# Optimization experiments

Measured on AMD Instinct MI355X. Metric: run time of the kernel, lower is better.

The kernel has to match this reference:

```python
import jax, jax.numpy as jnp
import numpy as np

B = 32768
INPUT_DIM = 2048
D = 2
HIDDEN = 128
V = 20          # output_dim (number of heads)
P = 6           # n_corr_params
R = 10          # r_lora = min(V // 2, 10)


def setup_inputs() -> dict:
    key = jax.random.key(0)
    ks = jax.random.split(key, 12)

    def lin(k, fan_in, shape):
        bound = 1.0 / np.sqrt(fan_in)
        return jax.random.uniform(k, shape, jnp.float32, -bound, bound)

    x = jax.random.normal(ks[0], (B, INPUT_DIM), jnp.float32)
    # encoder: Linear(input_dim, hidden) -> ReLU -> (Dropout=id) -> Linear(hidden, d)
    We1 = lin(ks[1], INPUT_DIM, (INPUT_DIM, HIDDEN))
    be1 = lin(ks[2], INPUT_DIM, (HIDDEN,))
    We2 = lin(ks[3], HIDDEN, (HIDDEN, D))
    be2 = lin(ks[4], HIDDEN, (D,))
    # 20 heads, each Linear(d, hidden) -> ReLU -> Linear(hidden, 6) -> Tanh,
    # stacked into batched weight tensors.
    W1 = lin(ks[5], D, (V, D, HIDDEN))
    b1 = lin(ks[6], D, (V, HIDDEN))
    W2 = lin(ks[7], HIDDEN, (V, HIDDEN, P))
    b2 = lin(ks[8], HIDDEN, (V, P))
    # LoRA params
    lora_A = jax.random.normal(ks[9], (D, R), jnp.float32) * 0.01
    lora_B = jax.random.normal(ks[10], (R, V * P), jnp.float32) * 0.01
    return {"x": x, "We1": We1, "be1": be1, "We2": We2, "be2": be2,
            "W1": W1, "b1": b1, "W2": W2, "b2": b2,
            "lora_A": lora_A, "lora_B": lora_B}


def reference(x, We1, be1, We2, be2, W1, b1, W2, b2, lora_A, lora_B):
    # encoder (nonlinear reduction; dropout is identity in eval)
    z = jax.nn.relu(x @ We1 + be1) @ We2 + be2            # [B, D]
    # all 20 heads as batched GEMMs
    h = jax.nn.relu(jnp.einsum('bd,vdh->bvh', z, W1) + b1)  # [B, V, HIDDEN]
    heads = jnp.tanh(jnp.einsum('bvh,vhp->bvp', h, W2) + b2)  # [B, V, P]
    # LoRA contribution, then outer tanh (note: double tanh, faithful to source)
    lora = (z @ lora_A @ lora_B).reshape(-1, V, P)         # [B, V, P]
    out = jnp.tanh(heads + 0.15 * lora)
    return (out, z)
```

## Files before the change

### kernel.cpp

```cpp
#include <hip/hip_runtime.h>
#include <hip/hip_bf16.h>
#include <cstdint>
#include <cstddef>

#define BDIM   32768
#define KDIM   2048
#define NDIM   128
#define VHEADS 20
#define PDIM   6
#define RLORA  10

#define BK      64
#define NCHUNK  (KDIM / BK)
#define OUT_ELEMS   (BDIM * VHEADS * PDIM)
#define WS_W_BYTES  (KDIM * NDIM * 2)

typedef __attribute__((ext_vector_type(8))) __bf16 bf16x8;
typedef __attribute__((ext_vector_type(4))) float f32x4;
typedef __attribute__((ext_vector_type(2))) float f32x2;
typedef __attribute__((ext_vector_type(4))) unsigned int u32x4;

union FragU { bf16x8 b; u32x4 u; };

__device__ __forceinline__ unsigned int cvt_pk_bf16(float lo, float hi) {
  unsigned int r;
  asm("v_cvt_pk_bf16_f32 %0, %1, %2" : "=v"(r) : "v"(lo), "v"(hi));
  return r;
}

__device__ __forceinline__ void gload_lds16(const void* g, void* l) {
  __builtin_amdgcn_global_load_lds(
      (const __attribute__((address_space(1))) void*)(g),
      (__attribute__((address_space(3))) void*)(l), 16, 0, 0);
}

__device__ __forceinline__ float fast_tanh(float x) {
  float ax = fabsf(x);
  float e  = __expf(-2.0f * ax);
  float t  = __fdividef(1.0f - e, 1.0f + e);
  return copysignf(t, x);
}

#define SBAR() __builtin_amdgcn_sched_barrier(0)
#define GL16(dst, addr, OFFSTR) \
  asm volatile("global_load_dwordx4 %0, %1, off offset:" OFFSTR \
               : "=v"(dst) : "v"(addr))

__global__ __launch_bounds__(256)
void k0_pack(const float* __restrict__ We1,
             const float* __restrict__ lA,
             const float* __restrict__ lB,
             unsigned short* __restrict__ wsw,
             float* __restrict__ wsM) {
  if (blockIdx.x == 128) {
    int t = threadIdx.x;
    if (t < 2 * VHEADS * PDIM) {
      int d  = t / (VHEADS * PDIM);
      int vp = t - d * (VHEADS * PDIM);
      float s = 0.f;
#pragma unroll
      for (int r = 0; r < RLORA; ++r)
        s = fmaf(lA[d * RLORA + r], lB[r * (VHEADS * PDIM) + vp], s);
      wsM[t] = s;
    }
    return;
  }
  int t    = blockIdx.x * 256 + threadIdx.x;
  int lane = t & 63;
  int blk  = t >> 6;
  int ks   = blk & 1;
  int nt   = (blk >> 1) & 7;
  int c    = blk >> 4;
  int n    = nt * 16 + (lane & 15);
  int kb   = c * 64 + ks * 32 + (lane >> 4) * 8;

  unsigned int u[4];
#pragma unroll
  for (int q = 0; q < 4; ++q) {
    float f0 = We1[(size_t)(kb + 2 * q + 0) * NDIM + n];
    float f1 = We1[(size_t)(kb + 2 * q + 1) * NDIM + n];
    __hip_bfloat16 h0 = __float2bfloat16(f0);
    __hip_bfloat16 h1 = __float2bfloat16(f1);
    u[q] = (unsigned int)*reinterpret_cast<unsigned short*>(&h0) |
           ((unsigned int)*reinterpret_cast<unsigned short*>(&h1) << 16);
  }
  *reinterpret_cast<u32x4*>(wsw + (size_t)t * 8) = u32x4{u[0], u[1], u[2], u[3]};
}

__global__ __launch_bounds__(512, 4)
void k1_fused(const float* __restrict__ x,
              const unsigned short* __restrict__ wp,
              const float* __restrict__ be1,
              const float* __restrict__ We2,
              const float* __restrict__ be2,
              const float* __restrict__ W1,
              const float* __restrict__ b1,
              const float* __restrict__ W2,
              const float* __restrict__ b2,
              const float* __restrict__ M,
              float* __restrict__ out,
              float* __restrict__ zout) {
  __shared__ char A0_[16384] __attribute__((aligned(16)));
  __shared__ char A1_[16384] __attribute__((aligned(16)));
  __shared__ float zpart2[64][2][2];
  __shared__ float zsh[64][2];

  const int tid  = threadIdx.x;
  const int lane = tid & 63;
  const int wv   = tid >> 6;
  const int wr   = wv & 3;
  const int wc   = wv >> 2;
  const int l15  = lane & 15;
  const int kgrp = lane >> 4;
  const int blk  = blockIdx.x;

  const char* bwave = (const char*)wp + wc * 8192 + lane * 16 + 4096;

  f32x4 acc[4];
#pragma unroll
  for (int i = 0; i < 4; ++i) acc[i] = f32x4{0.f, 0.f, 0.f, 0.f};

  auto STAGE_A = [&](char* Ad, int c) {
#pragma unroll
    for (int q = 0; q < 2; ++q) {
      int s = tid + q * 512;
      int row = s >> 4;
      int g = (s & 15) ^ (row & 7);
      const float* asrc = x + (size_t)(blk * 64 + row) * KDIM + c * BK + g * 4;
      gload_lds16(asrc, Ad + s * 16);
    }
  };

  FragU bE[8], bO[8];
  auto LOADB = [&](FragU* B, int c) {
    const char* p = bwave + (size_t)c * 16384;
    GL16(B[0].u, p, "-4096");
    GL16(B[1].u, p, "-3072");
    GL16(B[2].u, p, "-2048");
    GL16(B[3].u, p, "-1024");
    GL16(B[4].u, p, "0");
    GL16(B[5].u, p, "1024");
    GL16(B[6].u, p, "2048");
    GL16(B[7].u, p, "3072");
  };

  auto COMPUTE = [&](const char* Ad, const FragU* B) {
    const int row = wr * 16 + l15;
    const char* abase = Ad + row * 256;
    const int rx = (row & 7) << 4;
    f32x4 A0 = *(const f32x4*)(abase + (((kgrp * 2 + 0) << 4) ^ rx));
    f32x4 A1 = *(const f32x4*)(abase + (((kgrp * 2 + 1) << 4) ^ rx));
    f32x4 A2 = *(const f32x4*)(abase + 128 + (((kgrp * 2 + 0) << 4) ^ rx));
    f32x4 A3 = *(const f32x4*)(abase + 128 + (((kgrp * 2 + 1) << 4) ^ rx));
    FragU a0, a1;
    a0.u = u32x4{cvt_pk_bf16(A0.x, A0.y), cvt_pk_bf16(A0.z, A0.w),
                 cvt_pk_bf16(A1.x, A1.y), cvt_pk_bf16(A1.z, A1.w)};
    a1.u = u32x4{cvt_pk_bf16(A2.x, A2.y), cvt_pk_bf16(A2.z, A2.w),
                 cvt_pk_bf16(A3.x, A3.y), cvt_pk_bf16(A3.z, A3.w)};
    acc[0] = __builtin_amdgcn_mfma_f32_16x16x32_bf16(a0.b, B[0].b, acc[0], 0, 0, 0);
    acc[0] = __builtin_amdgcn_mfma_f32_16x16x32_bf16(a1.b, B[1].b, acc[0], 0, 0, 0);
    acc[1] = __builtin_amdgcn_mfma_f32_16x16x32_bf16(a0.b, B[2].b, acc[1], 0, 0, 0);
    acc[1] = __builtin_amdgcn_mfma_f32_16x16x32_bf16(a1.b, B[3].b, acc[1], 0, 0, 0);
    acc[2] = __builtin_amdgcn_mfma_f32_16x16x32_bf16(a0.b, B[4].b, acc[2], 0, 0, 0);
    acc[2] = __builtin_amdgcn_mfma_f32_16x16x32_bf16(a1.b, B[5].b, acc[2], 0, 0, 0);
    acc[3] = __builtin_amdgcn_mfma_f32_16x16x32_bf16(a0.b, B[6].b, acc[3], 0, 0, 0);
    acc[3] = __builtin_amdgcn_mfma_f32_16x16x32_bf16(a1.b, B[7].b, acc[3], 0, 0, 0);
  };

  STAGE_A(A0_, 0);
  LOADB(bE, 0);
  STAGE_A(A1_, 1);
  LOADB(bO, 1);

#pragma unroll 1
  for (int cc = 0; cc < NCHUNK / 2 - 1; ++cc) {
    asm volatile("s_waitcnt vmcnt(10)" ::: "memory");
    SBAR();
    __builtin_amdgcn_s_barrier();
    COMPUTE(A0_, bE);
    __builtin_amdgcn_s_barrier();
    SBAR();
    STAGE_A(A0_, 2 * cc + 2);
    LOADB(bE, 2 * cc + 2);
    asm volatile("s_waitcnt vmcnt(10)" ::: "memory");
    SBAR();
    __builtin_amdgcn_s_barrier();
    COMPUTE(A1_, bO);
    __builtin_amdgcn_s_barrier();
    SBAR();
    STAGE_A(A1_, 2 * cc + 3);
    LOADB(bO, 2 * cc + 3);
  }
  asm volatile("s_waitcnt vmcnt(10)" ::: "memory");
  SBAR();
  __builtin_amdgcn_s_barrier();
  COMPUTE(A0_, bE);
  asm volatile("s_waitcnt vmcnt(0)" ::: "memory");
  SBAR();
  __builtin_amdgcn_s_barrier();
  COMPUTE(A1_, bO);

  float part[4][2];
#pragma unroll
  for (int j = 0; j < 4; ++j) { part[j][0] = 0.f; part[j][1] = 0.f; }
#pragma unroll
  for (int nt = 0; nt < 4; ++nt) {
    int col = (wc * 4 + nt) * 16 + l15;
    float bb = be1[col];
    float w0 = We2[col * 2 + 0];
    float w1 = We2[col * 2 + 1];
#pragma unroll
    for (int j = 0; j < 4; ++j) {
      float h = acc[nt][j] + bb;
      h = h > 0.f ? h : 0.f;
      part[j][0] = fmaf(h, w0, part[j][0]);
      part[j][1] = fmaf(h, w1, part[j][1]);
    }
  }
#pragma unroll
  for (int m = 1; m < 16; m <<= 1) {
#pragma unroll
    for (int j = 0; j < 4; ++j) {
      part[j][0] += __shfl_xor(part[j][0], m, 64);
      part[j][1] += __shfl_xor(part[j][1], m, 64);
    }
  }
  if (l15 == 0) {
#pragma unroll
    for (int j = 0; j < 4; ++j) {
      int rl = wr * 16 + kgrp * 4 + j;
      zpart2[rl][wc][0] = part[j][0];
      zpart2[rl][wc][1] = part[j][1];
    }
  }
  __syncthreads();
  if (tid < 64) {
    float s0 = zpart2[tid][0][0] + zpart2[tid][1][0] + be2[0];
    float s1 = zpart2[tid][0][1] + zpart2[tid][1][1] + be2[1];
    zsh[tid][0] = s0;
    zsh[tid][1] = s1;
    f32x2 zz = {s0, s1};
    *(f32x2*)(zout + (size_t)(blk * 64 + tid) * 2) = zz;
  }
  __syncthreads();

  const int wvu = __builtin_amdgcn_readfirstlane(wv);
  float z0 = zsh[lane][0];
  float z1 = zsh[lane][1];
  float* orow = out + (size_t)(blk * 64 + lane) * (VHEADS * PDIM);

  auto head = [&](int v) {
    const float* w1a = W1 + (size_t)(v * 2 + 0) * NDIM;
    const float* w1b = W1 + (size_t)(v * 2 + 1) * NDIM;
    const float* bb1 = b1 + (size_t)v * NDIM;
    const float* w2  = W2 + (size_t)v * NDIM * PDIM;

    float p[6] = {0.f, 0.f, 0.f, 0.f, 0.f, 0.f};
#pragma unroll 4
    for (int h = 0; h < NDIM; ++h) {
      float hv = fmaf(z0, w1a[h], fmaf(z1, w1b[h], bb1[h]));
      hv = hv > 0.f ? hv : 0.f;
#pragma unroll
      for (int j = 0; j < 6; ++j) p[j] = fmaf(hv, w2[h * 6 + j], p[j]);
    }
    float o[6];
#pragma unroll
    for (int j = 0; j < 6; ++j) {
      float t1 = fast_tanh(p[j] + b2[v * PDIM + j]);
      float lo = fmaf(z0, M[v * PDIM + j], z1 * M[VHEADS * PDIM + v * PDIM + j]);
      o[j] = fast_tanh(fmaf(0.15f, lo, t1));
    }
    float* op = orow + v * PDIM;
    f32x2 o01 = {o[0], o[1]};
    f32x2 o23 = {o[2], o[3]};
    f32x2 o45 = {o[4], o[5]};
    __builtin_nontemporal_store(o01, (f32x2*)(op + 0));
    __builtin_nontemporal_store(o23, (f32x2*)(op + 2));
    __builtin_nontemporal_store(o45, (f32x2*)(op + 4));
  };

  head(wvu);
  head(wvu + 8);
  if (wvu < 4) head(wvu + 16);
}

extern "C" void kernel_launch(void* const* d_in, const int* in_sizes, int n_in,
                              void* d_out, int out_size, void* d_ws, size_t ws_size,
                              hipStream_t stream) {
  const float* x   = (const float*)d_in[0];
  const float* We1 = (const float*)d_in[1];
  const float* be1 = (const float*)d_in[2];
  const float* We2 = (const float*)d_in[3];
  const float* be2 = (const float*)d_in[4];
  const float* W1  = (const float*)d_in[5];
  const float* b1  = (const float*)d_in[6];
  const float* W2  = (const float*)d_in[7];
  const float* b2  = (const float*)d_in[8];
  const float* lA  = (const float*)d_in[9];
  const float* lB  = (const float*)d_in[10];

  float* out  = (float*)d_out;
  float* zout = out + OUT_ELEMS;
  unsigned short* wsw = (unsigned short*)d_ws;
  float* wsM = (float*)((char*)d_ws + WS_W_BYTES);

  hipLaunchKernelGGL(k0_pack, dim3(129), dim3(256), 0, stream,
                     We1, lA, lB, wsw, wsM);
  hipLaunchKernelGGL(k1_fused, dim3(BDIM / 64), dim3(512), 0, stream,
                     x, wsw, be1, We2, be2, W1, b1, W2, b2, wsM, out, zout);
}
```

Before: 99.55 us.

## Deepen A-tile LDS pipeline to four buffers with one barrier per chunk

Raises LDS staging of x tiles from two to four buffers, keeping A loads about three chunks ahead of compute. The trailing barrier after each compute is removed, so each chunk needs only one barrier, and the vmcnt waits are retuned to match. This targets memory latency stalls and barrier overhead in the memory-bound encoder GEMM. The cost is twice the LDS per block (64KB for A alone), which may lower occupancy from the launch-bounds target of 4 blocks per CU.

```diff
diff --git a/kernel.cpp b/kernel.cpp
--- a/kernel.cpp
+++ b/kernel.cpp
@@ -10,6 +10,7 @@
 #define PDIM   6
 #define RLORA  10
 
+#define BM      64
 #define BK      64
 #define NCHUNK  (KDIM / BK)
 #define OUT_ELEMS   (BDIM * VHEADS * PDIM)
@@ -102,6 +103,8 @@
               float* __restrict__ zout) {
   __shared__ char A0_[16384] __attribute__((aligned(16)));
   __shared__ char A1_[16384] __attribute__((aligned(16)));
+  __shared__ char A2_[16384] __attribute__((aligned(16)));
+  __shared__ char A3_[16384] __attribute__((aligned(16)));
   __shared__ float zpart2[64][2][2];
   __shared__ float zsh[64][2];
 
@@ -126,7 +129,7 @@
       int s = tid + q * 512;
       int row = s >> 4;
       int g = (s & 15) ^ (row & 7);
-      const float* asrc = x + (size_t)(blk * 64 + row) * KDIM + c * BK + g * 4;
+      const float* asrc = x + (size_t)(blk * BM + row) * KDIM + c * BK + g * 4;
       gload_lds16(asrc, Ad + s * 16);
     }
   };
@@ -167,38 +170,46 @@
     acc[3] = __builtin_amdgcn_mfma_f32_16x16x32_bf16(a1.b, B[7].b, acc[3], 0, 0, 0);
   };
 
+#define PH12(AB, BR, CB, AST, CA) do {                       \
+    asm volatile("s_waitcnt vmcnt(12)" ::: "memory");        \
+    SBAR();                                                  \
+    __builtin_amdgcn_s_barrier();                            \
+    COMPUTE(AB, BR);                                         \
+    SBAR();                                                  \
+    LOADB(BR, CB);                                           \
+    STAGE_A(AST, CA);                                        \
+  } while (0)
+
   STAGE_A(A0_, 0);
   LOADB(bE, 0);
   STAGE_A(A1_, 1);
   LOADB(bO, 1);
+  STAGE_A(A2_, 2);
 
 #pragma unroll 1
-  for (int cc = 0; cc < NCHUNK / 2 - 1; ++cc) {
-    asm volatile("s_waitcnt vmcnt(10)" ::: "memory");
-    SBAR();
-    __builtin_amdgcn_s_barrier();
-    COMPUTE(A0_, bE);
-    __builtin_amdgcn_s_barrier();
-    SBAR();
-    STAGE_A(A0_, 2 * cc + 2);
-    LOADB(bE, 2 * cc + 2);
-    asm volatile("s_waitcnt vmcnt(10)" ::: "memory");
-    SBAR();
-    __builtin_amdgcn_s_barrier();
-    COMPUTE(A1_, bO);
-    __builtin_amdgcn_s_barrier();
-    SBAR();
-    STAGE_A(A1_, 2 * cc + 3);
-    LOADB(bO, 2 * cc + 3);
-  }
+  for (int it = 0; it < 7; ++it) {
+    const int c = it * 4;
+    PH12(A0_, bE, c + 2, A3_, c + 3);
+    PH12(A1_, bO, c + 3, A0_, c + 4);
+    PH12(A2_, bE, c + 4, A1_, c + 5);
+    PH12(A3_, bO, c + 5, A2_, c + 6);
+  }
+  PH12(A0_, bE, 30, A3_, 31);
+  asm volatile("s_waitcnt vmcnt(12)" ::: "memory");
+  SBAR();
+  __builtin_amdgcn_s_barrier();
+  COMPUTE(A1_, bO);
+  SBAR();
+  LOADB(bO, 31);
   asm volatile("s_waitcnt vmcnt(10)" ::: "memory");
   SBAR();
   __builtin_amdgcn_s_barrier();
-  COMPUTE(A0_, bE);
+  COMPUTE(A2_, bE);
   asm volatile("s_waitcnt vmcnt(0)" ::: "memory");
   SBAR();
   __builtin_amdgcn_s_barrier();
-  COMPUTE(A1_, bO);
+  COMPUTE(A3_, bO);
+#undef PH12
 
   float part[4][2];
 #pragma unroll
@@ -234,20 +245,20 @@
     }
   }
   __syncthreads();
-  if (tid < 64) {
+  if (tid < BM) {
     float s0 = zpart2[tid][0][0] + zpart2[tid][1][0] + be2[0];
     float s1 = zpart2[tid][0][1] + zpart2[tid][1][1] + be2[1];
     zsh[tid][0] = s0;
     zsh[tid][1] = s1;
     f32x2 zz = {s0, s1};
-    *(f32x2*)(zout + (size_t)(blk * 64 + tid) * 2) = zz;
+    *(f32x2*)(zout + (size_t)(blk * BM + tid) * 2) = zz;
   }
   __syncthreads();
 
   const int wvu = __builtin_amdgcn_readfirstlane(wv);
   float z0 = zsh[lane][0];
   float z1 = zsh[lane][1];
-  float* orow = out + (size_t)(blk * 64 + lane) * (VHEADS * PDIM);
+  float* orow = out + (size_t)(blk * BM + lane) * (VHEADS * PDIM);
 
   auto head = [&](int v) {
     const float* w1a = W1 + (size_t)(v * 2 + 0) * NDIM;
@@ -306,6 +317,6 @@
 
   hipLaunchKernelGGL(k0_pack, dim3(129), dim3(256), 0, stream,
                      We1, lA, lB, wsw, wsM);
-  hipLaunchKernelGGL(k1_fused, dim3(BDIM / 64), dim3(512), 0, stream,
+  hipLaunchKernelGGL(k1_fused, dim3(BDIM / BM), dim3(512), 0, stream,
                      x, wsw, be1, We2, be2, W1, b1, W2, b2, wsM, out, zout);
 }
```

After: 113.3 us. +13.8%, slower.
